# Kernel optimization log

Measured on AMD Instinct MI355X. Metric: run time of the kernel, lower is better.

Reference implementation:

```python
import jax, jax.numpy as jnp
import numpy as np

EMB_DIM = 768
HEAD_SIZE = 64


def setup_inputs() -> dict:
    key = jax.random.key(0)
    kx, kk, kq, kv = jax.random.split(key, 4)
    B, S = 8, 2048
    bound = 1.0 / np.sqrt(EMB_DIM)  # torch Linear default init range
    x = jax.random.normal(kx, (B, S, EMB_DIM), dtype=jnp.float32)
    Wk = jax.random.uniform(kk, (EMB_DIM, HEAD_SIZE), jnp.float32, -bound, bound)
    Wq = jax.random.uniform(kq, (EMB_DIM, HEAD_SIZE), jnp.float32, -bound, bound)
    Wv = jax.random.uniform(kv, (EMB_DIM, HEAD_SIZE), jnp.float32, -bound, bound)
    return {"x": x, "Wk": Wk, "Wq": Wq, "Wv": Wv}


def reference(x, Wk, Wq, Wv):
    # bias-free projections: [b, s, d] @ [d, h] -> [b, s, h]
    key = jnp.einsum("bsd,dh->bsh", x, Wk)
    query = jnp.einsum("bsd,dh->bsh", x, Wq)
    value = jnp.einsum("bsd,dh->bsh", x, Wv)
    scale = 1.0 / jnp.sqrt(jnp.asarray(HEAD_SIZE, dtype=x.dtype))
    # [b, q, k] attention scores
    scores = jnp.einsum("bqh,bkh->bqk", query, key) * scale
    probs = jax.nn.softmax(scores, axis=-1)
    # weighted value sum: [b, q, h]
    out = jnp.einsum("bqk,bkh->bqh", probs, value)
    return out
```

## Files before the change

kernel.cpp:

```cpp
#include <hip/hip_runtime.h>
#include <hip/hip_bf16.h>
#include <stdint.h>

#define B_ 8
#define S_ 2048
#define D_ 768
#define H_ 64
#define M_ (B_*S_)

typedef __attribute__((ext_vector_type(8))) short bf16x8;
typedef __attribute__((ext_vector_type(4))) float f32x4;
typedef __attribute__((ext_vector_type(4))) float floatv4;
typedef __attribute__((ext_vector_type(4))) unsigned short u16x4;
typedef __attribute__((ext_vector_type(8))) unsigned short u16x8;

__device__ __forceinline__ uint16_t f2bf(float f) {
    union { float f; uint32_t u; } c; c.f = f;
    return (uint16_t)((c.u + 0x7FFFu + ((c.u >> 16) & 1u)) >> 16);
}

__device__ __forceinline__ void load_lds16(const void* g, void* l) {
    __builtin_amdgcn_global_load_lds(
        (const __attribute__((address_space(1))) uint32_t*)(const uint32_t*)g,
        (__attribute__((address_space(3))) uint32_t*)(uint32_t*)l,
        16, 0, 0);
}

__global__ __launch_bounds__(256) void k_convert_w(const float* __restrict__ Wk,
                                                   const float* __restrict__ Wq,
                                                   const float* __restrict__ Wv,
                                                   uint16_t* __restrict__ wt) {
    const int mat = blockIdx.y;
    const float* W = mat == 0 ? Wk : (mat == 1 ? Wq : Wv);
    const float scale = (mat == 1) ? 0.18033688011f : 1.0f;
    uint16_t* out = wt + (size_t)mat * (H_ * D_);
    int i = blockIdx.x * 256 + threadIdx.x;
    int d = i >> 6, h = i & 63;
    out[h * D_ + d] = f2bf(W[i] * scale);
}

__global__ __launch_bounds__(512, 2) void k_proj(const float* __restrict__ x,
                                                 const uint16_t* __restrict__ wt,
                                                 uint16_t* __restrict__ kb,
                                                 uint16_t* __restrict__ qb,
                                                 uint16_t* __restrict__ vt) {
    __shared__ char lds[65536];
    const int tid  = threadIdx.x;
    const int lane = tid & 63, wave = tid >> 6;
    const int l15  = lane & 15, g = lane >> 4;
    const int m0   = blockIdx.x * 64;
    const int mrow = (wave >> 1) * 16;
    const int nb   = (wave & 1) * 32;

    const int trow = tid >> 3, tc8 = tid & 7;
    const float* xrowp = x + (size_t)(m0 + trow) * D_ + tc8 * 8;
    const int xw = trow * 128 + ((tc8 ^ (trow & 7)) << 4);

    const int cswz = (((lane & 7) ^ (lane >> 3)) << 4);
    const char* wsrc[3];
    int wdst[3];
#pragma unroll
    for (int j = 0; j < 3; ++j) {
        int c = wave * 3 + j, mat = c >> 3, wrow = (c & 7) * 8 + (lane >> 3);
        wsrc[j] = (const char*)(wt + (size_t)mat * (H_ * D_) + (size_t)wrow * D_) + cswz;
        wdst[j] = 16384 + c * 1024;
    }

    floatv4 xr[12][2];
#pragma unroll
    for (int kt = 0; kt < 12; ++kt) {
        xr[kt][0] = *(const floatv4*)(xrowp + kt * 64);
        xr[kt][1] = *(const floatv4*)(xrowp + kt * 64 + 4);
    }

#pragma unroll
    for (int j = 0; j < 3; ++j)
        load_lds16(wsrc[j], lds + wdst[j]);
    {
        u16x8 cv;
        cv[0]=f2bf(xr[0][0][0]); cv[1]=f2bf(xr[0][0][1]); cv[2]=f2bf(xr[0][0][2]); cv[3]=f2bf(xr[0][0][3]);
        cv[4]=f2bf(xr[0][1][0]); cv[5]=f2bf(xr[0][1][1]); cv[6]=f2bf(xr[0][1][2]); cv[7]=f2bf(xr[0][1][3]);
        *(u16x8*)(lds + xw) = cv;
    }
    __syncthreads();

    f32x4 acc[3][2] = {};

#pragma unroll
    for (int kt = 0; kt < 12; ++kt) {
        const int cur = kt & 1, nxt = cur ^ 1;
        if (kt < 11) {
#pragma unroll
            for (int j = 0; j < 3; ++j)
                load_lds16(wsrc[j] + (size_t)(kt + 1) * 128, lds + nxt * 24576 + wdst[j]);
        }
        const char* xsb = lds + cur * 8192;
        const char* wsb = lds + 16384 + cur * 24576;
        bf16x8 a[2], b[3][2][2];
#pragma unroll
        for (int kk = 0; kk < 2; ++kk) {
            int row = mrow + l15;
            a[kk] = *(const bf16x8*)(xsb + row * 128 + ((kk*64 + g*16) ^ ((row & 7) << 4)));
        }
#pragma unroll
        for (int mat = 0; mat < 3; ++mat)
#pragma unroll
            for (int n = 0; n < 2; ++n)
#pragma unroll
                for (int kk = 0; kk < 2; ++kk) {
                    int row = nb + n * 16 + l15;
                    b[mat][n][kk] = *(const bf16x8*)(wsb + mat * 8192 + row * 128 +
                                                     ((kk*64 + g*16) ^ ((row & 7) << 4)));
                }
#pragma unroll
        for (int mat = 0; mat < 3; ++mat)
#pragma unroll
            for (int n = 0; n < 2; ++n)
#pragma unroll
                for (int kk = 0; kk < 2; ++kk)
                    acc[mat][n] = __builtin_amdgcn_mfma_f32_16x16x32_bf16(
                                      a[kk], b[mat][n][kk], acc[mat][n], 0, 0, 0);
        if (kt < 11) {
            u16x8 cv;
            cv[0]=f2bf(xr[kt+1][0][0]); cv[1]=f2bf(xr[kt+1][0][1]);
            cv[2]=f2bf(xr[kt+1][0][2]); cv[3]=f2bf(xr[kt+1][0][3]);
            cv[4]=f2bf(xr[kt+1][1][0]); cv[5]=f2bf(xr[kt+1][1][1]);
            cv[6]=f2bf(xr[kt+1][1][2]); cv[7]=f2bf(xr[kt+1][1][3]);
            *(u16x8*)(lds + nxt * 8192 + xw) = cv;
        }
        __syncthreads();
    }

#pragma unroll
    for (int mat = 0; mat < 3; ++mat)
#pragma unroll
        for (int n = 0; n < 2; ++n) {
            int col  = nb + n * 16 + l15;
            int row0 = m0 + mrow + g * 4;
            if (mat < 2) {
                uint16_t* out = (mat == 0) ? kb : qb;
#pragma unroll
                for (int r = 0; r < 4; ++r)
                    out[(size_t)(row0 + r) * H_ + col] = f2bf(acc[mat][n][r]);
            } else {
                int bb = row0 >> 11, s = row0 & 2047;
                u16x4 pk;
#pragma unroll
                for (int r = 0; r < 4; ++r) pk[r] = f2bf(acc[mat][n][r]);
                *(u16x4*)(vt + ((size_t)bb * H_ + col) * S_ + s) = pk;
            }
        }
}

__global__ __launch_bounds__(256) void k_attn(const uint16_t* __restrict__ qb,
                                              const uint16_t* __restrict__ kb,
                                              const uint16_t* __restrict__ vt,
                                              float* __restrict__ out) {
    __shared__ char plds[4][4096];
    __shared__ float o_buf[4 * 32 * 64];
    __shared__ float l_buf[4][32];
    const int tid  = threadIdx.x;
    const int lane = tid & 63, wave = tid >> 6;
    const int l15 = lane & 15, g = lane >> 4;
    const int batch = blockIdx.y;
    const int q0 = blockIdx.x * 32;
    const size_t qrow = (size_t)batch * S_ + q0;
    const float MBIAS = 4.0f;

    bf16x8 aq[2][2];
#pragma unroll
    for (int qm = 0; qm < 2; ++qm)
#pragma unroll
        for (int kk = 0; kk < 2; ++kk)
            aq[qm][kk] = *(const bf16x8*)(qb + (qrow + qm*16 + l15) * H_ + kk*32 + g*8);

    f32x4 o[2][4] = {};
    float Ls[2][4] = {};

    const uint16_t* kbase = kb + (size_t)batch * S_ * H_;
    const uint16_t* vbase = vt + (size_t)batch * H_ * S_;
    char* pl = plds[wave];
    const int kt0 = wave * 8;

    bf16x8 bk[4][2], bkn[4][2];
#pragma unroll
    for (int n = 0; n < 4; ++n)
#pragma unroll
        for (int kk = 0; kk < 2; ++kk)
            bk[n][kk] = *(const bf16x8*)(kbase + (size_t)(kt0*64 + n*16 + l15) * H_ + kk*32 + g*8);

#pragma unroll
    for (int j = 0; j < 8; ++j) {
        const int kt = kt0 + j;
        if (j < 7) {
#pragma unroll
            for (int n = 0; n < 4; ++n)
#pragma unroll
                for (int kk = 0; kk < 2; ++kk)
                    bkn[n][kk] = *(const bf16x8*)(kbase + (size_t)((kt+1)*64 + n*16 + l15) * H_ + kk*32 + g*8);
        }
        f32x4 s[2][4] = {};
#pragma unroll
        for (int qm = 0; qm < 2; ++qm)
#pragma unroll
            for (int n = 0; n < 4; ++n)
#pragma unroll
                for (int kk = 0; kk < 2; ++kk)
                    s[qm][n] = __builtin_amdgcn_mfma_f32_16x16x32_bf16(
                                   aq[qm][kk], bk[n][kk], s[qm][n], 0, 0, 0);

        bf16x8 bv[4][2];
#pragma unroll
        for (int nh = 0; nh < 4; ++nh)
#pragma unroll
            for (int kk = 0; kk < 2; ++kk)
                bv[nh][kk] = *(const bf16x8*)(vbase + (size_t)(nh*16 + l15) * S_ + kt*64 + kk*32 + g*8);

#pragma unroll
        for (int qm = 0; qm < 2; ++qm)
#pragma unroll
            for (int r = 0; r < 4; ++r) {
                int row = qm*16 + g*4 + r;
#pragma unroll
                for (int n = 0; n < 4; ++n) {
                    float p = exp2f(s[qm][n][r] - MBIAS);
                    Ls[qm][r] += p;
                    int cb  = ((n*16 + l15) * 2) ^ ((row & 7) << 4);
                    *(uint16_t*)(pl + row*128 + cb) = f2bf(p);
                }
            }

        bf16x8 pa[2][2];
#pragma unroll
        for (int qm = 0; qm < 2; ++qm)
#pragma unroll
            for (int kk = 0; kk < 2; ++kk) {
                int row = qm*16 + l15;
                int cb  = (kk*64 + g*16) ^ ((row & 7) << 4);
                pa[qm][kk] = *(const bf16x8*)(pl + row*128 + cb);
            }
#pragma unroll
        for (int qm = 0; qm < 2; ++qm)
#pragma unroll
            for (int nh = 0; nh < 4; ++nh)
#pragma unroll
                for (int kk = 0; kk < 2; ++kk)
                    o[qm][nh] = __builtin_amdgcn_mfma_f32_16x16x32_bf16(
                                    pa[qm][kk], bv[nh][kk], o[qm][nh], 0, 0, 0);
        if (j < 7) {
#pragma unroll
            for (int n = 0; n < 4; ++n)
#pragma unroll
                for (int kk = 0; kk < 2; ++kk)
                    bk[n][kk] = bkn[n][kk];
        }
    }

#pragma unroll
    for (int qm = 0; qm < 2; ++qm)
#pragma unroll
        for (int r = 0; r < 4; ++r) {
            float l = Ls[qm][r];
#pragma unroll
            for (int off = 1; off < 16; off <<= 1) l += __shfl_xor(l, off);
            Ls[qm][r] = l;
        }
    if (l15 == 0) {
#pragma unroll
        for (int qm = 0; qm < 2; ++qm)
#pragma unroll
            for (int r = 0; r < 4; ++r)
                l_buf[wave][qm*16 + g*4 + r] = Ls[qm][r];
    }
#pragma unroll
    for (int qm = 0; qm < 2; ++qm)
#pragma unroll
        for (int nh = 0; nh < 4; ++nh)
#pragma unroll
            for (int r = 0; r < 4; ++r) {
                int i = qm*16 + nh*4 + r;
                o_buf[(wave*32 + i)*64 + lane] = o[qm][nh][r];
            }
    __syncthreads();

    const int iw0 = wave * 8;
    const int qm0 = iw0 >> 4;
    float rinv[4];
#pragma unroll
    for (int r = 0; r < 4; ++r) {
        int row = qm0*16 + g*4 + r;
        rinv[r] = 1.0f / (l_buf[0][row] + l_buf[1][row] + l_buf[2][row] + l_buf[3][row]);
    }
    float* obase = out + qrow * H_;
#pragma unroll
    for (int ii = 0; ii < 8; ++ii) {
        int i = iw0 + ii;
        int nh = (i >> 2) & 3, r = i & 3;
        float tot = o_buf[(0*32 + i)*64 + lane] + o_buf[(1*32 + i)*64 + lane]
                  + o_buf[(2*32 + i)*64 + lane] + o_buf[(3*32 + i)*64 + lane];
        int row = qm0*16 + g*4 + r, col = nh*16 + l15;
        obase[(size_t)row * H_ + col] = tot * rinv[r];
    }
}

extern "C" void kernel_launch(void* const* d_in, const int* in_sizes, int n_in,
                              void* d_out, int out_size, void* d_ws, size_t ws_size,
                              hipStream_t stream) {
    const float* x  = (const float*)d_in[0];
    const float* Wk = (const float*)d_in[1];
    const float* Wq = (const float*)d_in[2];
    const float* Wv = (const float*)d_in[3];
    float* out = (float*)d_out;

    uint16_t* ws = (uint16_t*)d_ws;
    uint16_t* wt = ws;
    uint16_t* kb = wt + (size_t)3 * H_ * D_;
    uint16_t* qb = kb + (size_t)M_ * H_;
    uint16_t* vt = qb + (size_t)M_ * H_;

    k_convert_w<<<dim3(192, 3), dim3(256), 0, stream>>>(Wk, Wq, Wv, wt);
    k_proj<<<dim3(M_ / 64), dim3(512), 0, stream>>>(x, wt, kb, qb, vt);
    k_attn<<<dim3(S_ / 32, B_), dim3(256), 0, stream>>>(qb, kb, vt, out);
}
```

Before: 130.8 us.

## Split projection into small split-K blocks and widen attention to eight waves

The projection kernel now uses 16-row blocks of two waves that split the K dimension and read weights straight from global memory, with no LDS double buffering, and combines the two partial sums through LDS. The attention kernel goes from 4 to 8 waves per block, so each wave covers half as many key tiles. It uses a 1D grid that interleaves batches and merges the partial outputs with a two-stage LDS reduction. This trades fewer key tiles per wave for more reduction overhead, and the projection gives up LDS weight reuse in exchange for more, smaller blocks.

```diff
diff --git a/kernel.cpp b/kernel.cpp
--- a/kernel.cpp
+++ b/kernel.cpp
@@ -12,18 +12,10 @@
 typedef __attribute__((ext_vector_type(4))) float f32x4;
 typedef __attribute__((ext_vector_type(4))) float floatv4;
 typedef __attribute__((ext_vector_type(4))) unsigned short u16x4;
-typedef __attribute__((ext_vector_type(8))) unsigned short u16x8;
 
 __device__ __forceinline__ uint16_t f2bf(float f) {
     union { float f; uint32_t u; } c; c.f = f;
     return (uint16_t)((c.u + 0x7FFFu + ((c.u >> 16) & 1u)) >> 16);
-}
-
-__device__ __forceinline__ void load_lds16(const void* g, void* l) {
-    __builtin_amdgcn_global_load_lds(
-        (const __attribute__((address_space(1))) uint32_t*)(const uint32_t*)g,
-        (__attribute__((address_space(3))) uint32_t*)(uint32_t*)l,
-        16, 0, 0);
 }
 
 __global__ __launch_bounds__(256) void k_convert_w(const float* __restrict__ Wk,
@@ -39,134 +31,95 @@
     out[h * D_ + d] = f2bf(W[i] * scale);
 }
 
-__global__ __launch_bounds__(512, 2) void k_proj(const float* __restrict__ x,
-                                                 const uint16_t* __restrict__ wt,
-                                                 uint16_t* __restrict__ kb,
-                                                 uint16_t* __restrict__ qb,
-                                                 uint16_t* __restrict__ vt) {
-    __shared__ char lds[65536];
+__global__ __launch_bounds__(128) void k_proj(const float* __restrict__ x,
+                                              const uint16_t* __restrict__ wt,
+                                              uint16_t* __restrict__ kb,
+                                              uint16_t* __restrict__ qb,
+                                              uint16_t* __restrict__ vt) {
+    __shared__ float mbuf[12 * 4 * 64];
     const int tid  = threadIdx.x;
     const int lane = tid & 63, wave = tid >> 6;
     const int l15  = lane & 15, g = lane >> 4;
-    const int m0   = blockIdx.x * 64;
-    const int mrow = (wave >> 1) * 16;
-    const int nb   = (wave & 1) * 32;
-
-    const int trow = tid >> 3, tc8 = tid & 7;
-    const float* xrowp = x + (size_t)(m0 + trow) * D_ + tc8 * 8;
-    const int xw = trow * 128 + ((tc8 ^ (trow & 7)) << 4);
-
-    const int cswz = (((lane & 7) ^ (lane >> 3)) << 4);
-    const char* wsrc[3];
-    int wdst[3];
-#pragma unroll
-    for (int j = 0; j < 3; ++j) {
-        int c = wave * 3 + j, mat = c >> 3, wrow = (c & 7) * 8 + (lane >> 3);
-        wsrc[j] = (const char*)(wt + (size_t)mat * (H_ * D_) + (size_t)wrow * D_) + cswz;
-        wdst[j] = 16384 + c * 1024;
-    }
-
-    floatv4 xr[12][2];
-#pragma unroll
+    const int m0   = blockIdx.x * 16;
+
+    f32x4 acc[3][4] = {};
+
+    const float* xbase = x + (size_t)(m0 + l15) * D_ + g * 8 + wave * 384;
+
+#pragma unroll 2
     for (int kt = 0; kt < 12; ++kt) {
-        xr[kt][0] = *(const floatv4*)(xrowp + kt * 64);
-        xr[kt][1] = *(const floatv4*)(xrowp + kt * 64 + 4);
-    }
-
-#pragma unroll
-    for (int j = 0; j < 3; ++j)
-        load_lds16(wsrc[j], lds + wdst[j]);
-    {
-        u16x8 cv;
-        cv[0]=f2bf(xr[0][0][0]); cv[1]=f2bf(xr[0][0][1]); cv[2]=f2bf(xr[0][0][2]); cv[3]=f2bf(xr[0][0][3]);
-        cv[4]=f2bf(xr[0][1][0]); cv[5]=f2bf(xr[0][1][1]); cv[6]=f2bf(xr[0][1][2]); cv[7]=f2bf(xr[0][1][3]);
-        *(u16x8*)(lds + xw) = cv;
+        floatv4 a0 = *(const floatv4*)(xbase + kt * 32);
+        floatv4 a1 = *(const floatv4*)(xbase + kt * 32 + 4);
+        bf16x8 a;
+        a[0]=(short)f2bf(a0[0]); a[1]=(short)f2bf(a0[1]);
+        a[2]=(short)f2bf(a0[2]); a[3]=(short)f2bf(a0[3]);
+        a[4]=(short)f2bf(a1[0]); a[5]=(short)f2bf(a1[1]);
+        a[6]=(short)f2bf(a1[2]); a[7]=(short)f2bf(a1[3]);
+        const int k0 = wave * 384 + kt * 32 + g * 8;
+#pragma unroll
+        for (int mat = 0; mat < 3; ++mat)
+#pragma unroll
+            for (int cg = 0; cg < 4; ++cg) {
+                bf16x8 b = *(const bf16x8*)(wt + (size_t)mat * (H_ * D_) +
+                                            (size_t)(cg*16 + l15) * D_ + k0);
+                acc[mat][cg] = __builtin_amdgcn_mfma_f32_16x16x32_bf16(
+                                   a, b, acc[mat][cg], 0, 0, 0);
+            }
+    }
+
+    if (wave == 1) {
+#pragma unroll
+        for (int mat = 0; mat < 3; ++mat)
+#pragma unroll
+            for (int cg = 0; cg < 4; ++cg)
+#pragma unroll
+                for (int r = 0; r < 4; ++r)
+                    mbuf[((mat*4 + cg)*4 + r)*64 + lane] = acc[mat][cg][r];
     }
     __syncthreads();
-
-    f32x4 acc[3][2] = {};
-
-#pragma unroll
-    for (int kt = 0; kt < 12; ++kt) {
-        const int cur = kt & 1, nxt = cur ^ 1;
-        if (kt < 11) {
-#pragma unroll
-            for (int j = 0; j < 3; ++j)
-                load_lds16(wsrc[j] + (size_t)(kt + 1) * 128, lds + nxt * 24576 + wdst[j]);
-        }
-        const char* xsb = lds + cur * 8192;
-        const char* wsb = lds + 16384 + cur * 24576;
-        bf16x8 a[2], b[3][2][2];
-#pragma unroll
-        for (int kk = 0; kk < 2; ++kk) {
-            int row = mrow + l15;
-            a[kk] = *(const bf16x8*)(xsb + row * 128 + ((kk*64 + g*16) ^ ((row & 7) << 4)));
-        }
+    if (wave == 0) {
 #pragma unroll
         for (int mat = 0; mat < 3; ++mat)
 #pragma unroll
-            for (int n = 0; n < 2; ++n)
-#pragma unroll
-                for (int kk = 0; kk < 2; ++kk) {
-                    int row = nb + n * 16 + l15;
-                    b[mat][n][kk] = *(const bf16x8*)(wsb + mat * 8192 + row * 128 +
-                                                     ((kk*64 + g*16) ^ ((row & 7) << 4)));
+            for (int cg = 0; cg < 4; ++cg) {
+                int col  = cg*16 + l15;
+                int row0 = m0 + g * 4;
+                if (mat < 2) {
+                    uint16_t* out = (mat == 0) ? kb : qb;
+#pragma unroll
+                    for (int r = 0; r < 4; ++r) {
+                        float v = acc[mat][cg][r] + mbuf[((mat*4 + cg)*4 + r)*64 + lane];
+                        out[(size_t)(row0 + r) * H_ + col] = f2bf(v);
+                    }
+                } else {
+                    int bb = row0 >> 11, s = row0 & 2047;
+                    u16x4 pk;
+#pragma unroll
+                    for (int r = 0; r < 4; ++r)
+                        pk[r] = f2bf(acc[mat][cg][r] + mbuf[((mat*4 + cg)*4 + r)*64 + lane]);
+                    *(u16x4*)(vt + ((size_t)bb * H_ + col) * S_ + s) = pk;
                 }
-#pragma unroll
-        for (int mat = 0; mat < 3; ++mat)
-#pragma unroll
-            for (int n = 0; n < 2; ++n)
-#pragma unroll
-                for (int kk = 0; kk < 2; ++kk)
-                    acc[mat][n] = __builtin_amdgcn_mfma_f32_16x16x32_bf16(
-                                      a[kk], b[mat][n][kk], acc[mat][n], 0, 0, 0);
-        if (kt < 11) {
-            u16x8 cv;
-            cv[0]=f2bf(xr[kt+1][0][0]); cv[1]=f2bf(xr[kt+1][0][1]);
-            cv[2]=f2bf(xr[kt+1][0][2]); cv[3]=f2bf(xr[kt+1][0][3]);
-            cv[4]=f2bf(xr[kt+1][1][0]); cv[5]=f2bf(xr[kt+1][1][1]);
-            cv[6]=f2bf(xr[kt+1][1][2]); cv[7]=f2bf(xr[kt+1][1][3]);
-            *(u16x8*)(lds + nxt * 8192 + xw) = cv;
-        }
-        __syncthreads();
-    }
-
-#pragma unroll
-    for (int mat = 0; mat < 3; ++mat)
-#pragma unroll
-        for (int n = 0; n < 2; ++n) {
-            int col  = nb + n * 16 + l15;
-            int row0 = m0 + mrow + g * 4;
-            if (mat < 2) {
-                uint16_t* out = (mat == 0) ? kb : qb;
-#pragma unroll
-                for (int r = 0; r < 4; ++r)
-                    out[(size_t)(row0 + r) * H_ + col] = f2bf(acc[mat][n][r]);
-            } else {
-                int bb = row0 >> 11, s = row0 & 2047;
-                u16x4 pk;
-#pragma unroll
-                for (int r = 0; r < 4; ++r) pk[r] = f2bf(acc[mat][n][r]);
-                *(u16x4*)(vt + ((size_t)bb * H_ + col) * S_ + s) = pk;
-            }
-        }
-}
-
-__global__ __launch_bounds__(256) void k_attn(const uint16_t* __restrict__ qb,
-                                              const uint16_t* __restrict__ kb,
-                                              const uint16_t* __restrict__ vt,
-                                              float* __restrict__ out) {
-    __shared__ char plds[4][4096];
-    __shared__ float o_buf[4 * 32 * 64];
-    __shared__ float l_buf[4][32];
+            }
+    }
+}
+
+__global__ __launch_bounds__(512, 4) void k_attn(const uint16_t* __restrict__ qb,
+                                                 const uint16_t* __restrict__ kb,
+                                                 const uint16_t* __restrict__ vt,
+                                                 float* __restrict__ out) {
+    __shared__ char smem[66560];
     const int tid  = threadIdx.x;
     const int lane = tid & 63, wave = tid >> 6;
     const int l15 = lane & 15, g = lane >> 4;
-    const int batch = blockIdx.y;
-    const int q0 = blockIdx.x * 32;
+    const int bid = blockIdx.x;
+    const int batch = bid & 7;
+    const int q0 = (bid >> 3) * 32;
     const size_t qrow = (size_t)batch * S_ + q0;
     const float MBIAS = 4.0f;
 
+    float* o_buf4 = (float*)(smem + 32768);
+    float* l_buf  = (float*)(smem + 65536);
+
     bf16x8 aq[2][2];
 #pragma unroll
     for (int qm = 0; qm < 2; ++qm)
@@ -179,8 +132,8 @@
 
     const uint16_t* kbase = kb + (size_t)batch * S_ * H_;
     const uint16_t* vbase = vt + (size_t)batch * H_ * S_;
-    char* pl = plds[wave];
-    const int kt0 = wave * 8;
+    char* pl = smem + wave * 4096;
+    const int kt0 = wave * 4;
 
     bf16x8 bk[4][2], bkn[4][2];
 #pragma unroll
@@ -190,9 +143,9 @@
             bk[n][kk] = *(const bf16x8*)(kbase + (size_t)(kt0*64 + n*16 + l15) * H_ + kk*32 + g*8);
 
 #pragma unroll
-    for (int j = 0; j < 8; ++j) {
+    for (int j = 0; j < 4; ++j) {
         const int kt = kt0 + j;
-        if (j < 7) {
+        if (j < 3) {
 #pragma unroll
             for (int n = 0; n < 4; ++n)
 #pragma unroll
@@ -247,7 +200,7 @@
                 for (int kk = 0; kk < 2; ++kk)
                     o[qm][nh] = __builtin_amdgcn_mfma_f32_16x16x32_bf16(
                                     pa[qm][kk], bv[nh][kk], o[qm][nh], 0, 0, 0);
-        if (j < 7) {
+        if (j < 3) {
 #pragma unroll
             for (int n = 0; n < 4; ++n)
 #pragma unroll
@@ -263,43 +216,50 @@
             float l = Ls[qm][r];
 #pragma unroll
             for (int off = 1; off < 16; off <<= 1) l += __shfl_xor(l, off);
-            Ls[qm][r] = l;
+            if (l15 == 0) l_buf[wave*32 + qm*16 + g*4 + r] = l;
         }
-    if (l15 == 0) {
-#pragma unroll
-        for (int qm = 0; qm < 2; ++qm)
-#pragma unroll
-            for (int r = 0; r < 4; ++r)
-                l_buf[wave][qm*16 + g*4 + r] = Ls[qm][r];
-    }
-#pragma unroll
-    for (int qm = 0; qm < 2; ++qm)
-#pragma unroll
-        for (int nh = 0; nh < 4; ++nh)
-#pragma unroll
-            for (int r = 0; r < 4; ++r) {
-                int i = qm*16 + nh*4 + r;
-                o_buf[(wave*32 + i)*64 + lane] = o[qm][nh][r];
-            }
+
+    if (wave >= 4) {
+        float* dst = o_buf4 + (size_t)(wave - 4) * 32 * 64;
+#pragma unroll
+        for (int qm = 0; qm < 2; ++qm)
+#pragma unroll
+            for (int nh = 0; nh < 4; ++nh)
+#pragma unroll
+                for (int r = 0; r < 4; ++r)
+                    dst[(qm*16 + nh*4 + r)*64 + lane] = o[qm][nh][r];
+    }
     __syncthreads();
 
-    const int iw0 = wave * 8;
-    const int qm0 = iw0 >> 4;
-    float rinv[4];
-#pragma unroll
-    for (int r = 0; r < 4; ++r) {
-        int row = qm0*16 + g*4 + r;
-        rinv[r] = 1.0f / (l_buf[0][row] + l_buf[1][row] + l_buf[2][row] + l_buf[3][row]);
-    }
+    if (wave < 4) {
+        float* src = o_buf4 + (size_t)wave * 32 * 64;
+        float* dst = (float*)(smem + (size_t)wave * 8192);
+#pragma unroll
+        for (int qm = 0; qm < 2; ++qm)
+#pragma unroll
+            for (int nh = 0; nh < 4; ++nh)
+#pragma unroll
+                for (int r = 0; r < 4; ++r) {
+                    int i = qm*16 + nh*4 + r;
+                    dst[i*64 + lane] = o[qm][nh][r] + src[i*64 + lane];
+                }
+    }
+    __syncthreads();
+
     float* obase = out + qrow * H_;
 #pragma unroll
-    for (int ii = 0; ii < 8; ++ii) {
-        int i = iw0 + ii;
-        int nh = (i >> 2) & 3, r = i & 3;
-        float tot = o_buf[(0*32 + i)*64 + lane] + o_buf[(1*32 + i)*64 + lane]
-                  + o_buf[(2*32 + i)*64 + lane] + o_buf[(3*32 + i)*64 + lane];
-        int row = qm0*16 + g*4 + r, col = nh*16 + l15;
-        obase[(size_t)row * H_ + col] = tot * rinv[r];
+    for (int ii = 0; ii < 4; ++ii) {
+        int i = wave*4 + ii;
+        int qm = i >> 4, nh = (i >> 2) & 3, r = i & 3;
+        float tot = 0.f;
+#pragma unroll
+        for (int sl = 0; sl < 4; ++sl)
+            tot += ((float*)(smem + (size_t)sl * 8192))[i*64 + lane];
+        int row = qm*16 + g*4 + r, col = nh*16 + l15;
+        float L = 0.f;
+#pragma unroll
+        for (int wv = 0; wv < 8; ++wv) L += l_buf[wv*32 + row];
+        obase[(size_t)row * H_ + col] = tot / L;
     }
 }
 
@@ -319,6 +279,6 @@
     uint16_t* vt = qb + (size_t)M_ * H_;
 
     k_convert_w<<<dim3(192, 3), dim3(256), 0, stream>>>(Wk, Wq, Wv, wt);
-    k_proj<<<dim3(M_ / 64), dim3(512), 0, stream>>>(x, wt, kb, qb, vt);
-    k_attn<<<dim3(S_ / 32, B_), dim3(256), 0, stream>>>(qb, kb, vt, out);
-}
+    k_proj<<<dim3(M_ / 16), dim3(128), 0, stream>>>(x, wt, kb, qb, vt);
+    k_attn<<<dim3(512), dim3(512), 0, stream>>>(qb, kb, vt, out);
+}
```

After: 206.2 us. 1.58x slower.
